# Performance work log

Measured on AMD Instinct MI355X. Metric: run time of the kernel, lower is better.

## Reference

```python
import jax, jax.numpy as jnp
import numpy as np

N_NODES = 100000
N_EDGES = 1_600_000
IN_CH = 64
HID = 128
OUT_CH = 2


def _glorot(key, shape):
    fan_in = shape[0]
    return jax.random.normal(key, shape, dtype=jnp.float32) / jnp.sqrt(jnp.float32(fan_in))


def setup_inputs() -> dict:
    key = jax.random.key(0)
    ks = jax.random.split(key, 10)
    x = jax.random.normal(ks[0], (N_NODES, IN_CH), dtype=jnp.float32)
    edge_index = jax.random.randint(ks[1], (2, N_EDGES), 0, N_NODES, dtype=jnp.int64)
    # SAGEConv layer 0: lin_l (neighbor, with bias) + lin_r (root)
    W_n0 = _glorot(ks[2], (IN_CH, HID))
    W_s0 = _glorot(ks[3], (IN_CH, HID))
    b0 = jnp.zeros((HID,), dtype=jnp.float32)
    # SAGEConv layer 1
    W_n1 = _glorot(ks[4], (HID, HID))
    W_s1 = _glorot(ks[5], (HID, HID))
    b1 = jnp.zeros((HID,), dtype=jnp.float32)
    # final fc
    fc_w = _glorot(ks[6], (HID, OUT_CH))
    fc_b = jnp.zeros((OUT_CH,), dtype=jnp.float32)
    return {"x": x, "edge_index": edge_index, "W_n0": W_n0, "W_s0": W_s0, "b0": b0,
            "W_n1": W_n1, "W_s1": W_s1, "b1": b1, "fc_w": fc_w, "fc_b": fc_b}


def _sage_conv(h, src, dst, W_n, W_s, b, num_nodes):
    # mean aggregation of source features onto destination nodes
    agg = jax.ops.segment_sum(h[src], dst, num_segments=num_nodes)  # [N, d]
    cnt = jax.ops.segment_sum(jnp.ones_like(dst, dtype=h.dtype), dst, num_segments=num_nodes)
    mean = agg / jnp.maximum(cnt, 1.0)[:, None]
    return mean @ W_n + h @ W_s + b


def reference(x, edge_index, W_n0, W_s0, b0, W_n1, W_s1, b1, fc_w, fc_b):
    src, dst = edge_index[0], edge_index[1]
    n = x.shape[0]
    h = jax.nn.relu(_sage_conv(x, src, dst, W_n0, W_s0, b0, n))  # dropout is identity in eval mode
    h = jax.nn.relu(_sage_conv(h, src, dst, W_n1, W_s1, b1, n))
    return h @ fc_w + fc_b
```

## Files before the change

kernel.cpp:

```cpp
#include <hip/hip_runtime.h>

#define N_NODES 100000
#define IN_CH 64
#define HID 128
#define NBUCK ((N_NODES + 511) >> 9)
#define NCB 256

typedef short short8 __attribute__((ext_vector_type(8)));
typedef float floatx4 __attribute__((ext_vector_type(4)));
typedef float floatx2 __attribute__((ext_vector_type(2)));

__device__ __forceinline__ unsigned short f2bf(float f) {
    unsigned u = __builtin_bit_cast(unsigned, f);
    u += 0x7fffu + ((u >> 16) & 1u);
    return (unsigned short)(u >> 16);
}


__global__ __launch_bounds__(256) void hist_kernel(const int* __restrict__ dst,
                                                   int* __restrict__ table, int E, int chunk) {
    __shared__ int h[NBUCK];
    for (int i = threadIdx.x; i < NBUCK; i += 256) h[i] = 0;
    __syncthreads();
    int e0 = blockIdx.x * chunk;
    int e1 = min(E, e0 + chunk);
    for (int e = e0 + threadIdx.x; e < e1; e += 256) atomicAdd(&h[dst[e] >> 9], 1);
    __syncthreads();
    for (int i = threadIdx.x; i < NBUCK; i += 256) table[i * NCB + blockIdx.x] = h[i];
}

__global__ __launch_bounds__(256) void scanb1_kernel(int* __restrict__ table,
                                                     int* __restrict__ tot) {
    __shared__ int s[NCB];
    int b = blockIdx.x, t = threadIdx.x;
    int c = table[b * NCB + t];
    s[t] = c;
    __syncthreads();
#pragma unroll
    for (int off = 1; off < NCB; off <<= 1) {
        int v = (t >= off) ? s[t - off] : 0;
        __syncthreads();
        s[t] += v;
        __syncthreads();
    }
    table[b * NCB + t] = s[t] - c;
    if (t == NCB - 1) tot[b] = s[t];
}

__global__ __launch_bounds__(256) void scanb2_kernel(const int* __restrict__ tot,
                                                     int* __restrict__ bstart,
                                                     int* __restrict__ ptr, int E) {
    __shared__ int s[256];
    int t = threadIdx.x;
    int v = (t < NBUCK) ? tot[t] : 0;
    s[t] = v;
    __syncthreads();
#pragma unroll
    for (int off = 1; off < 256; off <<= 1) {
        int u = (t >= off) ? s[t - off] : 0;
        __syncthreads();
        s[t] += u;
        __syncthreads();
    }
    if (t < NBUCK) bstart[t] = s[t] - v;
    if (t == 0) {
        bstart[NBUCK] = E;
        ptr[N_NODES] = E;
    }
}

__global__ __launch_bounds__(256) void bin_kernel(const int* __restrict__ src,
                                                  const int* __restrict__ dst,
                                                  const int* __restrict__ table,
                                                  const int* __restrict__ bstart,
                                                  unsigned* __restrict__ binned, int E, int chunk) {
    __shared__ int cur[NBUCK];
    int blk = blockIdx.x;
    for (int i = threadIdx.x; i < NBUCK; i += 256) cur[i] = bstart[i] + table[i * NCB + blk];
    __syncthreads();
    int e0 = blk * chunk;
    int e1 = min(E, e0 + chunk);
    for (int e = e0 + threadIdx.x; e < e1; e += 256) {
        int d = dst[e];
        int b = d >> 9;
        int pos = atomicAdd(&cur[b], 1);
        binned[pos] = (unsigned)src[e] | ((unsigned)(d & 511) << 17);
    }
}

__global__ __launch_bounds__(256) void place_kernel(const unsigned* __restrict__ binned,
                                                    const int* __restrict__ bstart,
                                                    int* __restrict__ ptr,
                                                    int* __restrict__ sorted, int N) {
    __shared__ int deg[512];
    __shared__ int cur[512];
    __shared__ int ssum[256];
    int b = blockIdx.x, t = threadIdx.x;
    int start = bstart[b], end = bstart[b + 1];
    deg[t] = 0;
    deg[t + 256] = 0;
    __syncthreads();
    for (int i = start + t; i < end; i += 256) atomicAdd(&deg[binned[i] >> 17], 1);
    __syncthreads();
    int a = deg[2 * t], c = deg[2 * t + 1];
    int s2 = a + c;
    ssum[t] = s2;
    __syncthreads();
#pragma unroll
    for (int off = 1; off < 256; off <<= 1) {
        int u = (t >= off) ? ssum[t - off] : 0;
        __syncthreads();
        ssum[t] += u;
        __syncthreads();
    }
    int excl2 = ssum[t] - s2;
    cur[2 * t] = excl2;
    cur[2 * t + 1] = excl2 + a;
    int n0 = b * 512 + 2 * t;
    if (n0 < N) ptr[n0] = start + excl2;
    if (n0 + 1 < N) ptr[n0 + 1] = start + excl2 + a;
    __syncthreads();
    for (int i = start + t; i < end; i += 256) {
        unsigned p = binned[i];
        int dl = p >> 17;
        int pos = start + atomicAdd(&cur[dl], 1);
        sorted[pos] = (int)(p & 0x1FFFF);
    }
}

template <int K>
__device__ __forceinline__ void pack_dev(const float* __restrict__ Wn,
                                         const float* __restrict__ Ws,
                                         unsigned short* __restrict__ Bpack, int idx) {
    int s = idx >> 9;
    int rem = idx & 511;
    int t = rem >> 6;
    int lane = rem & 63;
    int quad = lane >> 4;
    int n = t * 16 + (lane & 15);
    unsigned short v[8];
#pragma unroll
    for (int j = 0; j < 8; ++j) {
        int k = s * 32 + quad * 8 + j;
        float w = (k < K) ? Wn[(size_t)k * HID + n] : Ws[(size_t)(k - K) * HID + n];
        v[j] = f2bf(w);
    }
    *(short8*)(Bpack + (size_t)idx * 8) = *(short8*)v;
}

__global__ __launch_bounds__(256) void prep_kernel(const float* __restrict__ x,
                                                   unsigned short* __restrict__ x_bf,
                                                   unsigned char* __restrict__ x_f8,
                                                   const float* __restrict__ Wn0,
                                                   const float* __restrict__ Ws0,
                                                   unsigned short* __restrict__ Bpack0,
                                                   const float* __restrict__ Wn1,
                                                   const float* __restrict__ Ws1,
                                                   unsigned short* __restrict__ Bpack1,
                                                   int n4) {
    int b = blockIdx.x;
    if (b < 8) {
        pack_dev<IN_CH>(Wn0, Ws0, Bpack0, b * 256 + threadIdx.x);
    } else if (b < 24) {
        pack_dev<HID>(Wn1, Ws1, Bpack1, (b - 8) * 256 + threadIdx.x);
    } else {
        int i = (b - 24) * 256 + threadIdx.x;
        if (i < n4) {
            float4 v = ((const float4*)x)[i];
            ushort4 o;
            o.x = f2bf(v.x); o.y = f2bf(v.y); o.z = f2bf(v.z); o.w = f2bf(v.w);
            ((ushort4*)x_bf)[i] = o;
            int p8 = __builtin_amdgcn_cvt_pk_fp8_f32(v.x, v.y, 0, false);
            p8 = __builtin_amdgcn_cvt_pk_fp8_f32(v.z, v.w, p8, true);
            ((unsigned*)x_f8)[i] = (unsigned)p8;
        }
    }
}

template <int C>
__global__ __launch_bounds__(256) void gather_mean_f8(const int* __restrict__ ptr,
                                                      const int* __restrict__ srcs,
                                                      const unsigned char* __restrict__ feat,
                                                      unsigned short* __restrict__ mean, int N) {
    constexpr int BPL = C / 16;
    constexpr int NA = BPL / 4;
    constexpr int G = 4;
    constexpr int STEP = 16;
    int w = (blockIdx.x * blockDim.x + threadIdx.x) >> 6;
    if (w >= N) return;
    int lane = threadIdx.x & 63;
    int g = lane >> 4;
    int l = lane & 15;
    int s0 = ptr[w], s1 = ptr[w + 1];
    int deg = s1 - s0;

    floatx2 acc2[2 * NA];
#pragma unroll
    for (int u = 0; u < 2 * NA; ++u) { acc2[u][0] = 0.0f; acc2[u][1] = 0.0f; }

    for (int jb = 0; jb < deg; jb += 64) {
        int rem = min(64, deg - jb);
        int idxreg = (jb + lane < deg) ? srcs[s0 + jb + lane] : 0;
        int fullend = rem & ~(STEP - 1);
        int o0 = 0;
        for (; o0 < fullend; o0 += STEP) {
            uint v[4][NA];
#pragma unroll
            for (int q = 0; q < 4; ++q) {
                int idx = __shfl(idxreg, o0 + q * G + g);
                if (NA == 2) {
                    uint2 t = *(const uint2*)(feat + (size_t)idx * C + l * 8);
                    v[q][0] = t.x; v[q][1] = t.y;
                } else {
                    v[q][0] = *(const unsigned*)(feat + (size_t)idx * C + l * 4);
                }
            }
#pragma unroll
            for (int q = 0; q < 4; ++q)
#pragma unroll
                for (int a = 0; a < NA; ++a) {
                    acc2[2 * a + 0] += __builtin_amdgcn_cvt_pk_f32_fp8(v[q][a], false);
                    acc2[2 * a + 1] += __builtin_amdgcn_cvt_pk_f32_fp8(v[q][a], true);
                }
        }
        if (o0 < rem) {
            uint v[4][NA];
#pragma unroll
            for (int q = 0; q < 4; ++q) {
                int o = o0 + q * G + g;
                int idx = __shfl(idxreg, o);
#pragma unroll
                for (int a = 0; a < NA; ++a) v[q][a] = 0;
                if (o < rem) {
                    if (NA == 2) {
                        uint2 t = *(const uint2*)(feat + (size_t)idx * C + l * 8);
                        v[q][0] = t.x; v[q][1] = t.y;
                    } else {
                        v[q][0] = *(const unsigned*)(feat + (size_t)idx * C + l * 4);
                    }
                }
            }
#pragma unroll
            for (int q = 0; q < 4; ++q)
#pragma unroll
                for (int a = 0; a < NA; ++a) {
                    acc2[2 * a + 0] += __builtin_amdgcn_cvt_pk_f32_fp8(v[q][a], false);
                    acc2[2 * a + 1] += __builtin_amdgcn_cvt_pk_f32_fp8(v[q][a], true);
                }
        }
    }
#pragma unroll
    for (int m = 16; m < 64; m <<= 1) {
#pragma unroll
        for (int u = 0; u < 2 * NA; ++u) {
            acc2[u][0] += __shfl_xor(acc2[u][0], m, 64);
            acc2[u][1] += __shfl_xor(acc2[u][1], m, 64);
        }
    }
    if (g == 0) {
        float inv = (deg > 0) ? 1.0f / (float)deg : 0.0f;
        unsigned short o[2 * BPL / 2];
#pragma unroll
        for (int u = 0; u < 2 * NA; ++u) {
            o[2 * u + 0] = f2bf(acc2[u][0] * inv);
            o[2 * u + 1] = f2bf(acc2[u][1] * inv);
        }
        if (NA == 2) *(uint4*)(mean + (size_t)w * C + l * 8) = *(const uint4*)o;
        else *(uint2*)(mean + (size_t)w * C + l * 4) = *(const uint2*)o;
    }
}

template <int KT, bool FUSE_FC>
__global__ __launch_bounds__(256) void sage_gemm_mfma(const unsigned short* __restrict__ meanb,
                                                      const unsigned short* __restrict__ hb,
                                                      const unsigned short* __restrict__ Bpack,
                                                      const float* __restrict__ bias,
                                                      const float* __restrict__ fcw,
                                                      const float* __restrict__ fcb,
                                                      unsigned short* __restrict__ outb,
                                                      unsigned char* __restrict__ out8,
                                                      float* __restrict__ outf, int N) {
    constexpr int KH = KT / 2;
    constexpr int LDA = KT + 8;
    __shared__ unsigned short As[64 * LDA];
    const int t = threadIdx.x;
    const int row0 = blockIdx.x * 64;

    constexpr int SEGS = KT / 8;
    for (int c = t; c < 64 * SEGS; c += 256) {
        int r = c / SEGS, seg = c % SEGS;
        int rsrc = row0 + r;
        if (rsrc >= N) rsrc = N - 1;
        const unsigned short* srcp = (seg < SEGS / 2)
                                         ? meanb + (size_t)rsrc * KH + seg * 8
                                         : hb + (size_t)rsrc * KH + (seg - SEGS / 2) * 8;
        *(uint4*)&As[r * LDA + seg * 8] = *(const uint4*)srcp;
    }
    __syncthreads();

    const int lane = t & 63;
    const int wave = t >> 6;
    const int quad = lane >> 4;
    const int lo = lane & 15;

    floatx4 acc[8];
#pragma unroll
    for (int i = 0; i < 8; ++i)
#pragma unroll
        for (int r = 0; r < 4; ++r) acc[i][r] = 0.0f;

    const unsigned short* abase = &As[(wave * 16 + lo) * LDA + quad * 8];
#pragma unroll
    for (int s = 0; s < KT / 32; ++s) {
        short8 a = *(const short8*)(abase + s * 32);
        const short8* bp = (const short8*)Bpack + (size_t)(s * 8) * 64 + lane;
#pragma unroll
        for (int tt = 0; tt < 8; ++tt) {
            short8 b = bp[tt * 64];
            acc[tt] = __builtin_amdgcn_mfma_f32_16x16x32_bf16(a, b, acc[tt], 0, 0, 0);
        }
    }

    if (!FUSE_FC) {
#pragma unroll
        for (int tt = 0; tt < 8; ++tt) {
            int col = tt * 16 + lo;
            float bv = bias[col];
#pragma unroll
            for (int r = 0; r < 4; ++r) {
                int row = row0 + wave * 16 + quad * 4 + r;
                if (row < N) {
                    float v = fmaxf(acc[tt][r] + bv, 0.0f);
                    outb[(size_t)row * HID + col] = f2bf(v);
                    int p8 = __builtin_amdgcn_cvt_pk_fp8_f32(v, v, 0, false);
                    out8[(size_t)row * HID + col] = (unsigned char)(p8 & 0xff);
                }
            }
        }
    } else {
        float o0[4] = {}, o1[4] = {};
#pragma unroll
        for (int tt = 0; tt < 8; ++tt) {
            int col = tt * 16 + lo;
            float bv = bias[col];
            float w0 = fcw[col * 2 + 0];
            float w1 = fcw[col * 2 + 1];
#pragma unroll
            for (int r = 0; r < 4; ++r) {
                float v = fmaxf(acc[tt][r] + bv, 0.0f);
                o0[r] += v * w0;
                o1[r] += v * w1;
            }
        }
#pragma unroll
        for (int r = 0; r < 4; ++r) {
#pragma unroll
            for (int m = 8; m >= 1; m >>= 1) {
                o0[r] += __shfl_xor(o0[r], m, 16);
                o1[r] += __shfl_xor(o1[r], m, 16);
            }
        }
        if (lo == 0) {
#pragma unroll
            for (int r = 0; r < 4; ++r) {
                int row = row0 + wave * 16 + quad * 4 + r;
                if (row < N) {
                    outf[(size_t)row * 2 + 0] = o0[r] + fcb[0];
                    outf[(size_t)row * 2 + 1] = o1[r] + fcb[1];
                }
            }
        }
    }
}

extern "C" void kernel_launch(void* const* d_in, const int* in_sizes, int n_in,
                              void* d_out, int out_size, void* d_ws, size_t ws_size,
                              hipStream_t stream) {
    const float* x   = (const float*)d_in[0];
    const int*   ei  = (const int*)d_in[1];
    const float* Wn0 = (const float*)d_in[2];
    const float* Ws0 = (const float*)d_in[3];
    const float* b0  = (const float*)d_in[4];
    const float* Wn1 = (const float*)d_in[5];
    const float* Ws1 = (const float*)d_in[6];
    const float* b1  = (const float*)d_in[7];
    const float* fcw = (const float*)d_in[8];
    const float* fcb = (const float*)d_in[9];
    float* out = (float*)d_out;

    const int E = in_sizes[1] / 2;
    const int* src = ei;
    const int* dst = ei + E;
    const int N = N_NODES;
    const int chunk = (E + NCB - 1) / NCB;

    char* ws = (char*)d_ws;
    size_t off = 0;
    int* table  = (int*)(ws + off); off += (size_t)NBUCK * NCB * 4;
    int* tot    = (int*)(ws + off); off += 4096;
    int* bstart = (int*)(ws + off); off += 4096;
    int* ptr    = (int*)(ws + off); off += (size_t)(N + 1) * 4 + 60; off &= ~(size_t)63;
    unsigned* binned = (unsigned*)(ws + off); off += (size_t)E * 4;
    int* sorted = (int*)(ws + off); off += (size_t)E * 4;
    off = (off + 255) & ~(size_t)255;
    unsigned short* x_bf   = (unsigned short*)(ws + off); off += (size_t)N * IN_CH * 2;
    unsigned short* mean0  = (unsigned short*)(ws + off); off += (size_t)N * IN_CH * 2;
    unsigned short* h1_bf  = (unsigned short*)(ws + off); off += (size_t)N * HID * 2;
    unsigned short* mean1  = (unsigned short*)(ws + off); off += (size_t)N * HID * 2;
    unsigned char*  h1_f8  = (unsigned char*)(ws + off);  off += (size_t)N * HID;
    unsigned char*  x_f8   = (unsigned char*)(ws + off);  off += (size_t)N * IN_CH;
    off = (off + 255) & ~(size_t)255;
    unsigned short* Bpack0 = (unsigned short*)(ws + off); off += (size_t)(2 * IN_CH / 32) * 8 * 64 * 8 * 2;
    unsigned short* Bpack1 = (unsigned short*)(ws + off); off += (size_t)(2 * HID / 32) * 8 * 64 * 8 * 2;

    hist_kernel<<<NCB, 256, 0, stream>>>(dst, table, E, chunk);
    scanb1_kernel<<<NBUCK, 256, 0, stream>>>(table, tot);
    scanb2_kernel<<<1, 256, 0, stream>>>(tot, bstart, ptr, E);
    bin_kernel<<<NCB, 256, 0, stream>>>(src, dst, table, bstart, binned, E, chunk);
    place_kernel<<<NBUCK, 256, 0, stream>>>(binned, bstart, ptr, sorted, N);

    {
        int n4 = N * IN_CH / 4;
        prep_kernel<<<24 + (n4 + 255) / 256, 256, 0, stream>>>(x, x_bf, x_f8, Wn0, Ws0, Bpack0,
                                                               Wn1, Ws1, Bpack1, n4);
    }

    gather_mean_f8<IN_CH><<<(N * 64 + 255) / 256, 256, 0, stream>>>(ptr, sorted, x_f8, mean0, N);
    sage_gemm_mfma<2 * IN_CH, false><<<(N + 63) / 64, 256, 0, stream>>>(
        mean0, x_bf, Bpack0, b0, nullptr, nullptr, h1_bf, h1_f8, nullptr, N);

    gather_mean_f8<HID><<<(N * 64 + 255) / 256, 256, 0, stream>>>(ptr, sorted, h1_f8, mean1, N);
    sage_gemm_mfma<2 * HID, true><<<(N + 63) / 64, 256, 0, stream>>>(
        mean1, h1_bf, Bpack1, b1, fcw, fcb, nullptr, nullptr, out, N);
}
```

Measured before the change: 266.7 us.

## Fuse neighbor mean gather into SAGE GEMM kernels and merge histogram with prep

Each SAGE layer now gathers the fp8 neighbor features straight into the GEMM's LDS tile, one wave handling 16 rows, rather than writing a bf16 mean buffer to global memory and reading it back. The edge histogram is merged into the prep kernel, removing one launch. This saves the global round trip and two launches. The cost is that each GEMM block now does gather work serially per wave before the MFMA stage, with lower occupancy from the larger LDS tile and less latency hiding for the irregular loads.

```diff
diff --git a/kernel.cpp b/kernel.cpp
--- a/kernel.cpp
+++ b/kernel.cpp
@@ -16,18 +16,6 @@
     return (unsigned short)(u >> 16);
 }
 
-
-__global__ __launch_bounds__(256) void hist_kernel(const int* __restrict__ dst,
-                                                   int* __restrict__ table, int E, int chunk) {
-    __shared__ int h[NBUCK];
-    for (int i = threadIdx.x; i < NBUCK; i += 256) h[i] = 0;
-    __syncthreads();
-    int e0 = blockIdx.x * chunk;
-    int e1 = min(E, e0 + chunk);
-    for (int e = e0 + threadIdx.x; e < e1; e += 256) atomicAdd(&h[dst[e] >> 9], 1);
-    __syncthreads();
-    for (int i = threadIdx.x; i < NBUCK; i += 256) table[i * NCB + blockIdx.x] = h[i];
-}
 
 __global__ __launch_bounds__(256) void scanb1_kernel(int* __restrict__ table,
                                                      int* __restrict__ tot) {
@@ -148,23 +136,34 @@
     *(short8*)(Bpack + (size_t)idx * 8) = *(short8*)v;
 }
 
-__global__ __launch_bounds__(256) void prep_kernel(const float* __restrict__ x,
-                                                   unsigned short* __restrict__ x_bf,
-                                                   unsigned char* __restrict__ x_f8,
-                                                   const float* __restrict__ Wn0,
-                                                   const float* __restrict__ Ws0,
-                                                   unsigned short* __restrict__ Bpack0,
-                                                   const float* __restrict__ Wn1,
-                                                   const float* __restrict__ Ws1,
-                                                   unsigned short* __restrict__ Bpack1,
-                                                   int n4) {
+__global__ __launch_bounds__(256) void histprep_kernel(const int* __restrict__ dst,
+                                                       int* __restrict__ table, int E, int chunk,
+                                                       const float* __restrict__ x,
+                                                       unsigned short* __restrict__ x_bf,
+                                                       unsigned char* __restrict__ x_f8,
+                                                       const float* __restrict__ Wn0,
+                                                       const float* __restrict__ Ws0,
+                                                       unsigned short* __restrict__ Bpack0,
+                                                       const float* __restrict__ Wn1,
+                                                       const float* __restrict__ Ws1,
+                                                       unsigned short* __restrict__ Bpack1,
+                                                       int n4) {
     int b = blockIdx.x;
-    if (b < 8) {
-        pack_dev<IN_CH>(Wn0, Ws0, Bpack0, b * 256 + threadIdx.x);
-    } else if (b < 24) {
-        pack_dev<HID>(Wn1, Ws1, Bpack1, (b - 8) * 256 + threadIdx.x);
+    if (b < NCB) {
+        __shared__ int h[NBUCK];
+        for (int i = threadIdx.x; i < NBUCK; i += 256) h[i] = 0;
+        __syncthreads();
+        int e0 = b * chunk;
+        int e1 = min(E, e0 + chunk);
+        for (int e = e0 + threadIdx.x; e < e1; e += 256) atomicAdd(&h[dst[e] >> 9], 1);
+        __syncthreads();
+        for (int i = threadIdx.x; i < NBUCK; i += 256) table[i * NCB + b] = h[i];
+    } else if (b < NCB + 8) {
+        pack_dev<IN_CH>(Wn0, Ws0, Bpack0, (b - NCB) * 256 + threadIdx.x);
+    } else if (b < NCB + 24) {
+        pack_dev<HID>(Wn1, Ws1, Bpack1, (b - NCB - 8) * 256 + threadIdx.x);
     } else {
-        int i = (b - 24) * 256 + threadIdx.x;
+        int i = (b - NCB - 24) * 256 + threadIdx.x;
         if (i < n4) {
             float4 v = ((const float4*)x)[i];
             ushort4 o;
@@ -178,20 +177,17 @@
 }
 
 template <int C>
-__global__ __launch_bounds__(256) void gather_mean_f8(const int* __restrict__ ptr,
-                                                      const int* __restrict__ srcs,
-                                                      const unsigned char* __restrict__ feat,
-                                                      unsigned short* __restrict__ mean, int N) {
-    constexpr int BPL = C / 16;
-    constexpr int NA = BPL / 4;
-    constexpr int G = 4;
-    constexpr int STEP = 16;
-    int w = (blockIdx.x * blockDim.x + threadIdx.x) >> 6;
-    if (w >= N) return;
-    int lane = threadIdx.x & 63;
+__device__ __forceinline__ void gather_node_lds(const int* __restrict__ ptr,
+                                                const int* __restrict__ srcs,
+                                                const unsigned char* __restrict__ feat,
+                                                int node, int N,
+                                                unsigned short* __restrict__ lds_row,
+                                                int lane) {
+    constexpr int NA = C / 64;
     int g = lane >> 4;
     int l = lane & 15;
-    int s0 = ptr[w], s1 = ptr[w + 1];
+    int nclamp = min(node, N - 1);
+    int s0 = ptr[nclamp], s1 = ptr[nclamp + 1];
     int deg = s1 - s0;
 
     floatx2 acc2[2 * NA];
@@ -201,16 +197,16 @@
     for (int jb = 0; jb < deg; jb += 64) {
         int rem = min(64, deg - jb);
         int idxreg = (jb + lane < deg) ? srcs[s0 + jb + lane] : 0;
-        int fullend = rem & ~(STEP - 1);
+        int fullend = rem & ~15;
         int o0 = 0;
-        for (; o0 < fullend; o0 += STEP) {
+        for (; o0 < fullend; o0 += 16) {
             uint v[4][NA];
 #pragma unroll
             for (int q = 0; q < 4; ++q) {
-                int idx = __shfl(idxreg, o0 + q * G + g);
+                int idx = __shfl(idxreg, o0 + q * 4 + g);
                 if (NA == 2) {
-                    uint2 t = *(const uint2*)(feat + (size_t)idx * C + l * 8);
-                    v[q][0] = t.x; v[q][1] = t.y;
+                    uint2 tt = *(const uint2*)(feat + (size_t)idx * C + l * 8);
+                    v[q][0] = tt.x; v[q][1] = tt.y;
                 } else {
                     v[q][0] = *(const unsigned*)(feat + (size_t)idx * C + l * 4);
                 }
@@ -227,14 +223,14 @@
             uint v[4][NA];
 #pragma unroll
             for (int q = 0; q < 4; ++q) {
-                int o = o0 + q * G + g;
+                int o = o0 + q * 4 + g;
                 int idx = __shfl(idxreg, o);
 #pragma unroll
                 for (int a = 0; a < NA; ++a) v[q][a] = 0;
                 if (o < rem) {
                     if (NA == 2) {
-                        uint2 t = *(const uint2*)(feat + (size_t)idx * C + l * 8);
-                        v[q][0] = t.x; v[q][1] = t.y;
+                        uint2 tt = *(const uint2*)(feat + (size_t)idx * C + l * 8);
+                        v[q][0] = tt.x; v[q][1] = tt.y;
                     } else {
                         v[q][0] = *(const unsigned*)(feat + (size_t)idx * C + l * 4);
                     }
@@ -259,47 +255,50 @@
     }
     if (g == 0) {
         float inv = (deg > 0) ? 1.0f / (float)deg : 0.0f;
-        unsigned short o[2 * BPL / 2];
+        unsigned short o[4 * NA];
 #pragma unroll
         for (int u = 0; u < 2 * NA; ++u) {
             o[2 * u + 0] = f2bf(acc2[u][0] * inv);
             o[2 * u + 1] = f2bf(acc2[u][1] * inv);
         }
-        if (NA == 2) *(uint4*)(mean + (size_t)w * C + l * 8) = *(const uint4*)o;
-        else *(uint2*)(mean + (size_t)w * C + l * 4) = *(const uint2*)o;
+        if (NA == 2) *(uint4*)(lds_row + l * 8) = *(const uint4*)o;
+        else *(uint2*)(lds_row + l * 4) = *(const uint2*)o;
     }
 }
 
 template <int KT, bool FUSE_FC>
-__global__ __launch_bounds__(256) void sage_gemm_mfma(const unsigned short* __restrict__ meanb,
-                                                      const unsigned short* __restrict__ hb,
-                                                      const unsigned short* __restrict__ Bpack,
-                                                      const float* __restrict__ bias,
-                                                      const float* __restrict__ fcw,
-                                                      const float* __restrict__ fcb,
-                                                      unsigned short* __restrict__ outb,
-                                                      unsigned char* __restrict__ out8,
-                                                      float* __restrict__ outf, int N) {
+__global__ __launch_bounds__(256) void sage_fused(const int* __restrict__ ptr,
+                                                  const int* __restrict__ srcs,
+                                                  const unsigned char* __restrict__ feat8,
+                                                  const unsigned short* __restrict__ hb,
+                                                  const unsigned short* __restrict__ Bpack,
+                                                  const float* __restrict__ bias,
+                                                  const float* __restrict__ fcw,
+                                                  const float* __restrict__ fcb,
+                                                  unsigned short* __restrict__ outb,
+                                                  unsigned char* __restrict__ out8,
+                                                  float* __restrict__ outf, int N) {
     constexpr int KH = KT / 2;
     constexpr int LDA = KT + 8;
     __shared__ unsigned short As[64 * LDA];
     const int t = threadIdx.x;
     const int row0 = blockIdx.x * 64;
-
-    constexpr int SEGS = KT / 8;
-    for (int c = t; c < 64 * SEGS; c += 256) {
-        int r = c / SEGS, seg = c % SEGS;
-        int rsrc = row0 + r;
-        if (rsrc >= N) rsrc = N - 1;
-        const unsigned short* srcp = (seg < SEGS / 2)
-                                         ? meanb + (size_t)rsrc * KH + seg * 8
-                                         : hb + (size_t)rsrc * KH + (seg - SEGS / 2) * 8;
-        *(uint4*)&As[r * LDA + seg * 8] = *(const uint4*)srcp;
-    }
-    __syncthreads();
-
     const int lane = t & 63;
     const int wave = t >> 6;
+
+    constexpr int HSEG = KH / 8;
+    for (int c = t; c < 64 * HSEG; c += 256) {
+        int r = c / HSEG, seg = c % HSEG;
+        int rsrc = min(row0 + r, N - 1);
+        *(uint4*)&As[r * LDA + KH + seg * 8] = *(const uint4*)(hb + (size_t)rsrc * KH + seg * 8);
+    }
+
+    for (int i = 0; i < 16; ++i) {
+        int r = wave * 16 + i;
+        gather_node_lds<KH>(ptr, srcs, feat8, row0 + r, N, &As[r * LDA], lane);
+    }
+    __syncthreads();
+
     const int quad = lane >> 4;
     const int lo = lane & 15;
 
@@ -404,32 +403,27 @@
     int* sorted = (int*)(ws + off); off += (size_t)E * 4;
     off = (off + 255) & ~(size_t)255;
     unsigned short* x_bf   = (unsigned short*)(ws + off); off += (size_t)N * IN_CH * 2;
-    unsigned short* mean0  = (unsigned short*)(ws + off); off += (size_t)N * IN_CH * 2;
     unsigned short* h1_bf  = (unsigned short*)(ws + off); off += (size_t)N * HID * 2;
-    unsigned short* mean1  = (unsigned short*)(ws + off); off += (size_t)N * HID * 2;
     unsigned char*  h1_f8  = (unsigned char*)(ws + off);  off += (size_t)N * HID;
     unsigned char*  x_f8   = (unsigned char*)(ws + off);  off += (size_t)N * IN_CH;
     off = (off + 255) & ~(size_t)255;
     unsigned short* Bpack0 = (unsigned short*)(ws + off); off += (size_t)(2 * IN_CH / 32) * 8 * 64 * 8 * 2;
     unsigned short* Bpack1 = (unsigned short*)(ws + off); off += (size_t)(2 * HID / 32) * 8 * 64 * 8 * 2;
 
-    hist_kernel<<<NCB, 256, 0, stream>>>(dst, table, E, chunk);
+    {
+        int n4 = N * IN_CH / 4;
+        int nblk = NCB + 24 + (n4 + 255) / 256;
+        histprep_kernel<<<nblk, 256, 0, stream>>>(dst, table, E, chunk, x, x_bf, x_f8,
+                                                  Wn0, Ws0, Bpack0, Wn1, Ws1, Bpack1, n4);
+    }
     scanb1_kernel<<<NBUCK, 256, 0, stream>>>(table, tot);
     scanb2_kernel<<<1, 256, 0, stream>>>(tot, bstart, ptr, E);
     bin_kernel<<<NCB, 256, 0, stream>>>(src, dst, table, bstart, binned, E, chunk);
     place_kernel<<<NBUCK, 256, 0, stream>>>(binned, bstart, ptr, sorted, N);
 
-    {
-        int n4 = N * IN_CH / 4;
-        prep_kernel<<<24 + (n4 + 255) / 256, 256, 0, stream>>>(x, x_bf, x_f8, Wn0, Ws0, Bpack0,
-                                                               Wn1, Ws1, Bpack1, n4);
-    }
-
-    gather_mean_f8<IN_CH><<<(N * 64 + 255) / 256, 256, 0, stream>>>(ptr, sorted, x_f8, mean0, N);
-    sage_gemm_mfma<2 * IN_CH, false><<<(N + 63) / 64, 256, 0, stream>>>(
-        mean0, x_bf, Bpack0, b0, nullptr, nullptr, h1_bf, h1_f8, nullptr, N);
-
-    gather_mean_f8<HID><<<(N * 64 + 255) / 256, 256, 0, stream>>>(ptr, sorted, h1_f8, mean1, N);
-    sage_gemm_mfma<2 * HID, true><<<(N + 63) / 64, 256, 0, stream>>>(
-        mean1, h1_bf, Bpack1, b1, fcw, fcb, nullptr, nullptr, out, N);
-}
+    sage_fused<2 * IN_CH, false><<<(N + 63) / 64, 256, 0, stream>>>(
+        ptr, sorted, x_f8, x_bf, Bpack0, b0, nullptr, nullptr, h1_bf, h1_f8, nullptr, N);
+
+    sage_fused<2 * HID, true><<<(N + 63) / 64, 256, 0, stream>>>(
+        ptr, sorted, h1_f8, h1_bf, Bpack1, b1, fcw, fcb, nullptr, nullptr, out, N);
+}
```

Result: slower. 287.1 us (+7.6%).
